# Kernel optimization log

Measured on AMD Instinct MI355X. Metric: run time of the kernel, lower is better.

The kernel has to match this reference:

```python
import jax, jax.numpy as jnp
import numpy as np

# --- static config matching init_kwargs ---
L = 6            # discretization level -> 2^L Euler substeps per unit time
T = 10           # number of time units
N = 1000         # number of particles
DX = 16          # state dim (== obs dim)
INIT_VAL = 0.0
SUB = 2 ** L
HL = 2.0 ** (-L)
S = SUB * T + 1  # total path length


def setup_inputs() -> dict:
    key = jax.random.key(0)
    k1, k2, k3, k4 = jax.random.split(key, 4)
    input_path = jax.random.normal(k1, (S, DX), dtype=jnp.float32) * 0.1
    observe_path = jax.random.normal(k2, (T + 1, DX), dtype=jnp.float32) * 0.5
    # stable linear drift mu(x) = x @ A.T, constant diffusion matrix Sig
    A = (-0.5 * jnp.eye(DX) + 0.05 * jax.random.normal(k3, (DX, DX))).astype(jnp.float32)
    Sig = (0.3 * jnp.eye(DX) + 0.02 * jax.random.normal(k4, (DX, DX))).astype(jnp.float32)
    return {"input_path": input_path, "observe_path": observe_path, "A": A, "Sig": Sig}


def _mu(x, A):
    return x @ A.T


def _llg(x, y):
    # Gaussian observation log-likelihood per particle: x (N,DX), y (DX,)
    return -0.5 * jnp.sum((y - x) ** 2, axis=-1)


def _euler_segment(x0, A, Sig, key):
    # unit_path_update: 2^L Euler-Maruyama steps; returns (SUB, N, DX)
    dw = jax.random.normal(key, (SUB, x0.shape[0], DX)) * np.sqrt(HL).astype(np.float32)
    def step(x, d):
        xn = x + _mu(x, A) * HL + d @ Sig.T
        return xn, xn
    _, seg = jax.lax.scan(step, x0, dw)
    return seg


def _multinomial_idx(wn, dice):
    bins = jnp.cumsum(wn)
    bins = bins.at[-1].set(jnp.maximum(1.0, bins[-1]))  # bins[-1] = max(1, bins[-1])
    return jnp.clip(jnp.searchsorted(bins, dice, side="right"), 0, N - 1)


def _forward(input_path, observe_path, A, Sig):
    key = jax.random.key(42)
    un = jnp.full((S, N, DX), INIT_VAL, dtype=input_path.dtype)
    un_hat = jnp.full((S, N, DX), INIT_VAL, dtype=input_path.dtype)
    gn = jnp.zeros((N,), dtype=input_path.dtype)
    wn = jnp.full((N,), 1.0 / N, dtype=input_path.dtype)
    for t in range(T):  # static unroll over time units (indices are static)
        start, upd = SUB * t, SUB * (t + 1)
        kdw = jax.random.fold_in(key, 2 * t)
        kres = jax.random.fold_in(key, 2 * t + 1)
        un = un.at[: start + 1].set(un_hat[: start + 1])
        seg = _euler_segment(un[start], A, Sig, kdw)
        un = un.at[start + 1 : upd + 1].set(seg)
        un = un.at[:, -1, :].set(input_path)  # pin conditioned path as last particle
        gn = _llg(un[upd], observe_path[t + 1]) + gn
        wn = jax.nn.softmax(gn)  # exp(gn - max)/sum, numerically stable
        ess = 1.0 / jnp.sum(wn ** 2)
        do_rs = ess <= N / 2
        idx = _multinomial_idx(wn, jax.random.uniform(kres, (N,)))
        prefix = un[: upd + 1]
        gathered = prefix[:, idx, :]
        new_prefix = jnp.where(do_rs, gathered, prefix)
        gn = jnp.where(do_rs, jnp.zeros_like(gn), gn)
        un_hat = un_hat.at[: upd + 1].set(new_prefix)
        un_hat = un_hat.at[:, -1, :].set(input_path)
    # sample_output: draw one particle index from final weights
    kfin = jax.random.fold_in(key, 2 * T)
    i0 = _multinomial_idx(wn, jax.random.uniform(kfin, (1,)))[0]
    return un[:, i0, :]  # (S, DX)


def reference(input_path, observe_path, A, Sig):
    return _forward(input_path, observe_path, A, Sig)
```

## Files before the change

### kernel.cpp

```cpp
#include <hip/hip_runtime.h>
#include <cstdint>
#include <cstddef>

#pragma clang fp contract(off)


typedef unsigned int u32;

#define NP   1000
#define DXC  16
#define SUBC 64
#define TC   10
#define SC   641

#define WS_XS   0
#define WS_ANC  160000
#define WS_LIN  170000
#define WS_XF0  170032
#define WS_XF1  186032
#define WS_GN0  202032
#define WS_GN1  203032
#define WS_DSG  204032

__device__ __forceinline__ u32 rotl32(u32 v, u32 d) { return (v << d) | (v >> (32u - d)); }

__device__ __forceinline__ void tf2x32(u32 k0, u32 k1, u32 c0, u32 c1, u32& o0, u32& o1) {
  u32 ks0 = k0, ks1 = k1, ks2 = k0 ^ k1 ^ 0x1BD11BDAu;
  u32 x0 = c0 + ks0, x1 = c1 + ks1;
  x0 += x1; x1 = rotl32(x1,13); x1 ^= x0;
  x0 += x1; x1 = rotl32(x1,15); x1 ^= x0;
  x0 += x1; x1 = rotl32(x1,26); x1 ^= x0;
  x0 += x1; x1 = rotl32(x1, 6); x1 ^= x0;
  x0 += ks1; x1 += ks2 + 1u;
  x0 += x1; x1 = rotl32(x1,17); x1 ^= x0;
  x0 += x1; x1 = rotl32(x1,29); x1 ^= x0;
  x0 += x1; x1 = rotl32(x1,16); x1 ^= x0;
  x0 += x1; x1 = rotl32(x1,24); x1 ^= x0;
  x0 += ks2; x1 += ks0 + 2u;
  x0 += x1; x1 = rotl32(x1,13); x1 ^= x0;
  x0 += x1; x1 = rotl32(x1,15); x1 ^= x0;
  x0 += x1; x1 = rotl32(x1,26); x1 ^= x0;
  x0 += x1; x1 = rotl32(x1, 6); x1 ^= x0;
  x0 += ks0; x1 += ks1 + 3u;
  x0 += x1; x1 = rotl32(x1,17); x1 ^= x0;
  x0 += x1; x1 = rotl32(x1,29); x1 ^= x0;
  x0 += x1; x1 = rotl32(x1,16); x1 ^= x0;
  x0 += x1; x1 = rotl32(x1,24); x1 ^= x0;
  x0 += ks1; x1 += ks2 + 4u;
  x0 += x1; x1 = rotl32(x1,13); x1 ^= x0;
  x0 += x1; x1 = rotl32(x1,15); x1 ^= x0;
  x0 += x1; x1 = rotl32(x1,26); x1 ^= x0;
  x0 += x1; x1 = rotl32(x1, 6); x1 ^= x0;
  x0 += ks2; x1 += ks0 + 5u;
  o0 = x0; o1 = x1;
}

__device__ __forceinline__ u32 bits32p(u32 k0, u32 k1, u32 i) {
  u32 o0, o1; tf2x32(k0, k1, 0u, i, o0, o1); return o0 ^ o1;
}

__device__ __forceinline__ float u01(u32 b) {
  return __uint_as_float((b >> 9) | 0x3f800000u) - 1.0f;
}

__device__ __forceinline__ float xla_exp(float input) {
#pragma clang fp contract(off)
  float x = fminf(input, 88.3762626647950f);
  x = fmaxf(x, -88.3762626647949f);
  float fx = floorf(__builtin_fmaf(x, 1.44269504088896341f, 0.5f));
  float tmp = 0.693359375f * fx;
  float z0  = -2.12194440e-4f * fx;
  float xr = x - tmp;
  xr = xr - z0;
  float z = xr * xr;
  float y = __builtin_fmaf(xr, 1.9875691500e-4f, 1.3981999507e-3f);
  y = __builtin_fmaf(y, xr, 8.3334519073e-3f);
  y = __builtin_fmaf(y, xr, 4.1665795894e-2f);
  y = __builtin_fmaf(y, xr, 1.6666665459e-1f);
  y = __builtin_fmaf(y, xr, 5.0000001201e-1f);
  y = __builtin_fmaf(y, z, xr);
  y = 1.0f + y;
  int n = (int)fx;
  float p2n = __uint_as_float((u32)(n + 127) << 23);
  float res = y * p2n;
  return fmaxf(res, input);
}

__device__ __forceinline__ float xla_log(float input) {
#pragma clang fp contract(off)
  float t0 = fmaxf(input, __uint_as_float(0x00800000u));
  u32 bi = __float_as_uint(t0);
  float e = (float)(int)((bi >> 23) - 126u);
  float x = __uint_as_float((bi & 0x807fffffu) | 0x3f000000u);
  float mo, mx;
  if (x < 0.707106781186547524f) { mx = x; mo = 1.0f; } else { mx = 0.0f; mo = 0.0f; }
  x = x - 1.0f;
  e = e - mo;
  x = x + mx;
  float z = x * x;
  float y = __builtin_fmaf(x, 7.0376836292e-2f, -1.1514610310e-1f);
  y = __builtin_fmaf(y, x, 1.1676998740e-1f);
  y = __builtin_fmaf(y, x, -1.2420140846e-1f);
  y = __builtin_fmaf(y, x, 1.4249322787e-1f);
  y = __builtin_fmaf(y, x, -1.6668057665e-1f);
  y = __builtin_fmaf(y, x, 2.0000714765e-1f);
  y = __builtin_fmaf(y, x, -2.4999993993e-1f);
  y = __builtin_fmaf(y, x, 3.3333331174e-1f);
  y = y * x;
  y = y * z;
  y = __builtin_fmaf(e, -2.12194440e-4f, y);
  y = y - 0.5f * z;
  x = x + y;
  x = __builtin_fmaf(e, 0.693359375f, x);
  return x;
}

__device__ __forceinline__ float xla_log1p(float x) {
#pragma clang fp contract(off)
  float ax = fabsf(x);
  if (ax < 1e-4f) {
    float t = (-0.5f * x) + 1.0f;
    return t * x;
  }
  return xla_log(x + 1.0f);
}

__device__ __forceinline__ float xla_erfinv(float u) {
#pragma clang fp contract(off)
  float w = -xla_log1p((-u) * u);
  float p;
  if (w < 5.0f) {
    float ww = w - 2.5f;
    p = 2.81022636e-08f;
    p = 3.43273939e-07f  + p * ww;
    p = -3.5233877e-06f  + p * ww;
    p = -4.39150654e-06f + p * ww;
    p = 0.00021858087f   + p * ww;
    p = -0.00125372503f  + p * ww;
    p = -0.00417768164f  + p * ww;
    p = 0.246640727f     + p * ww;
    p = 1.50140941f      + p * ww;
  } else {
    float ww = (float)__builtin_sqrt((double)w) - 3.0f;
    p = -0.000200214257f;
    p = 0.000100950558f + p * ww;
    p = 0.00134934322f  + p * ww;
    p = -0.00367342844f + p * ww;
    p = 0.00573950773f  + p * ww;
    p = -0.0076224613f  + p * ww;
    p = 0.00943887047f  + p * ww;
    p = 1.00167406f     + p * ww;
    p = 2.83297682f     + p * ww;
  }
  return p * u;
}

#define U_LO __uint_as_float(0xBF7FFFFFu)

__device__ __forceinline__ float nrm(u32 bits) {
#pragma clang fp contract(off)
  float f = u01(bits);
  float u = (f * 2.0f) + U_LO;
  u = fmaxf(U_LO, u);
  return __uint_as_float(0x3FB504F3u) * xla_erfinv(u);
}

__global__ __launch_bounds__(512, 1) void k_gen(const float* __restrict__ Sg,
                                                float* __restrict__ wsf) {
#pragma clang fp contract(off)
  __shared__ float Sg_s[256];
  int tid = threadIdx.x;
  if (tid < 256) Sg_s[tid] = Sg[tid];
  __syncthreads();
  int gtid = (int)blockIdx.x * 512 + tid;
  int nl = gtid & 7;
  int s  = (gtid >> 3) & 63;
  int q  = gtid >> 9;
  int t  = q / 125, blk = q - t * 125;
  int n  = blk * 8 + nl;
  u32 k0, k1; tf2x32(0u, 42u, 0u, (u32)(2 * t), k0, k1);
  float dwv[DXC];
#pragma unroll
  for (int k = 0; k < DXC; ++k) {
    u32 b = bits32p(k0, k1, (u32)(s * 16000 + n * 16 + k));
    dwv[k] = nrm(b) * 0.125f;
  }
  float* dst = wsf + WS_DSG + (size_t)gtid * 16;
#pragma unroll
  for (int d = 0; d < DXC; ++d) {
    float dg = 0.0f;
#pragma unroll
    for (int k = 0; k < DXC; ++k) dg = __builtin_fmaf(dwv[k], Sg_s[d * 16 + k], dg);
    dst[d] = dg;
  }
}

__device__ void cumsum_tree_par(const float* x0, float* out0, float* scr, int tid) {
#pragma clang fp contract(off)
  const int nlv[10] = {1000, 500, 250, 125, 62, 31, 15, 7, 3, 1};
  const float* raw[10]; float* scn[10]; float* rawm[10];
  raw[0] = x0; scn[0] = out0;
  int off = 0;
  for (int k = 1; k < 10; ++k) {
    rawm[k] = scr + off; raw[k] = rawm[k]; off += nlv[k];
    scn[k] = scr + off; off += nlv[k];
  }
  for (int k = 0; k < 9; ++k) {
    int nr = nlv[k + 1];
    for (int i = tid; i < nr; i += 512) rawm[k + 1][i] = raw[k][2 * i] + raw[k][2 * i + 1];
    __syncthreads();
  }
  if (tid == 0) scn[9][0] = raw[9][0];
  __syncthreads();
  for (int k = 8; k >= 0; --k) {
    int nk = nlv[k], nr = nlv[k + 1];
    if (tid == 0) scn[k][0] = raw[k][0];
    for (int i = tid; i < nr; i += 512) scn[k][2 * i + 1] = scn[k + 1][i];
    if ((nk & 1) == 0) {
      for (int i = 1 + tid; i < nr; i += 512) scn[k][2 * i] = scn[k + 1][i - 1] + raw[k][2 * i];
    } else {
      for (int i = 1 + tid; i <= nr; i += 512) scn[k][2 * i] = scn[k + 1][i - 1] + raw[k][2 * i];
    }
    __syncthreads();
  }
}

__device__ void filter_step(int s, const float* __restrict__ inp,
                            const float* __restrict__ obs,
                            float* __restrict__ wsf, int tid, int wr,
                            float* gn_s, float* e_s, float* wn_s, float* bins_s,
                            float* scr_s, float* red_s, int* src_s, float* sh) {
#pragma clang fp contract(off)
  const float* XFp = wsf + ((s & 1) ? WS_XF1 : WS_XF0);
  const float* GNp = wsf + (((s & 1) ^ 1) ? WS_GN1 : WS_GN0);
  float* GNw = wsf + ((s & 1) ? WS_GN1 : WS_GN0);
  int* ANC = (int*)(wsf + WS_ANC);
  int upd = SUBC * (s + 1);

  for (int n = tid; n < NP; n += 512) {
    float sacc = 0.0f;
    for (int d = 0; d < DXC; ++d) {
      float fv = (n == NP - 1) ? inp[upd * 16 + d] : XFp[n * 16 + d];
      float dd = obs[(s + 1) * 16 + d] - fv;
      float sq = dd * dd;
      sacc = sacc + sq;
    }
    float gp = (s == 0) ? 0.0f : GNp[n];
    gn_s[n] = (-0.5f * sacc) + gp;
  }
  __syncthreads();
  {
    float mv = -__builtin_inff();
    for (int n = tid; n < NP; n += 512) mv = fmaxf(mv, gn_s[n]);
#pragma unroll
    for (int off = 32; off >= 1; off >>= 1) mv = fmaxf(mv, __shfl_xor(mv, off));
    if ((tid & 63) == 0) red_s[tid >> 6] = mv;
    __syncthreads();
    if (tid == 0) {
      float a = fmaxf(fmaxf(red_s[0], red_s[1]), fmaxf(red_s[2], red_s[3]));
      float b = fmaxf(fmaxf(red_s[4], red_s[5]), fmaxf(red_s[6], red_s[7]));
      sh[0] = fmaxf(a, b);
    }
    __syncthreads();
  }
  float m = sh[0];
  for (int n = tid; n < NP; n += 512) e_s[n] = xla_exp(gn_s[n] - m);
  __syncthreads();
  if (tid < 8) {
    float a = 0.0f;
    for (int i = 0; i < 125; ++i) a = a + e_s[i * 8 + tid];
    red_s[tid] = a;
  }
  __syncthreads();
  if (tid == 0) {
    float b0 = red_s[0] + red_s[4], b1 = red_s[1] + red_s[5],
          b2 = red_s[2] + red_s[6], b3 = red_s[3] + red_s[7];
    float c0 = b0 + b2, c1 = b1 + b3;
    sh[1] = c0 + c1;
  }
  __syncthreads();
  float ssum = sh[1];
  for (int n = tid; n < NP; n += 512) wn_s[n] = e_s[n] / ssum;
  __syncthreads();
  if (tid < 8) {
    float a = 0.0f;
    for (int i = 0; i < 125; ++i) { float v = wn_s[i * 8 + tid]; float q = v * v; a = a + q; }
    red_s[tid] = a;
  }
  __syncthreads();
  if (tid == 0) {
    float b0 = red_s[0] + red_s[4], b1 = red_s[1] + red_s[5],
          b2 = red_s[2] + red_s[6], b3 = red_s[3] + red_s[7];
    float c0 = b0 + b2, c1 = b1 + b3;
    float ss = c0 + c1;
    float ess = 1.0f / ss;
    sh[2] = (ess <= 500.0f) ? 1.0f : 0.0f;
  }
  __syncthreads();
  cumsum_tree_par(wn_s, bins_s, scr_s, tid);
  if (tid == 0) bins_s[NP - 1] = fmaxf(1.0f, bins_s[NP - 1]);
  __syncthreads();
  int rs = (sh[2] != 0.0f);
  u32 kr0, kr1; tf2x32(0u, 42u, 0u, (u32)(2 * s + 1), kr0, kr1);
  for (int n = tid; n < NP; n += 512) {
    u32 b = bits32p(kr0, kr1, (u32)n);
    float dice = fmaxf(0.0f, u01(b));
    int lo = 0, hi = NP;
    while (lo < hi) { int mid = (lo + hi) >> 1; if (bins_s[mid] <= dice) lo = mid + 1; else hi = mid; }
    int idx = lo > NP - 1 ? NP - 1 : lo;
    int a = rs ? idx : n;
    src_s[n] = (n == NP - 1) ? (NP - 1) : a;
    if (wr) {
      ANC[s * NP + n] = a;
      GNw[n] = rs ? 0.0f : gn_s[n];
    }
  }
  __syncthreads();
}

__global__ __launch_bounds__(512, 1) void k_step(const float* __restrict__ inp,
                                                 const float* __restrict__ obs,
                                                 const float* __restrict__ A,
                                                 float* __restrict__ wsf, int t) {
#pragma clang fp contract(off)
  __shared__ float dsg_s[8192];
  __shared__ float gn_s[NP], e_s[NP], wn_s[NP], bins_s[NP], scr_s[2048];
  __shared__ float red_s[8], sh[4];
  __shared__ int src_s[NP];
  int tid = threadIdx.x;
  int base = (int)blockIdx.x * 8;
  const float* DSG = wsf + WS_DSG + (size_t)t * 1024000 + (size_t)blockIdx.x * 8192;
#pragma unroll
  for (int j = 0; j < 16; ++j) dsg_s[j * 512 + tid] = DSG[j * 512 + tid];
  if (t > 0) {
    filter_step(t - 1, inp, obs, wsf, tid, blockIdx.x == 0,
                gn_s, e_s, wn_s, bins_s, scr_s, red_s, src_s, sh);
  } else {
    __syncthreads();
  }
  if (tid < 128) {
    int p = tid >> 4, d = tid & 15;
    int n = base + p;
    float Ar[DXC];
#pragma unroll
    for (int k = 0; k < DXC; ++k) Ar[k] = A[d * 16 + k];
    float x = 0.0f;
    if (t > 0) {
      const float* XFp = wsf + (((t - 1) & 1) ? WS_XF1 : WS_XF0);
      int s0 = src_s[n];
      x = (s0 == NP - 1) ? inp[(SUBC * t) * 16 + d] : XFp[s0 * 16 + d];
    }
    wsf[WS_XS + t * 16000 + n * 16 + d] = x;
    for (int sl = 0; sl < SUBC; ++sl) {
      float mu = 0.0f;
#pragma unroll
      for (int k = 0; k < DXC; ++k) {
        float xk = __shfl(x, k, 16);
        mu = __builtin_fmaf(xk, Ar[k], mu);
      }
      float t2 = x + mu * 0.015625f;
      x = t2 + dsg_s[sl * 128 + p * 16 + d];
    }
    float* XFc = wsf + ((t & 1) ? WS_XF1 : WS_XF0);
    XFc[n * 16 + d] = x;
  }
}

__global__ __launch_bounds__(512, 1) void k_fin(const float* __restrict__ inp,
                                                const float* __restrict__ obs,
                                                float* __restrict__ wsf) {
#pragma clang fp contract(off)
  __shared__ float gn_s[NP], e_s[NP], wn_s[NP], bins_s[NP], scr_s[2048];
  __shared__ float red_s[8], sh[4];
  __shared__ int src_s[NP];
  int tid = threadIdx.x;
  filter_step(TC - 1, inp, obs, wsf, tid, 0,
              gn_s, e_s, wn_s, bins_s, scr_s, red_s, src_s, sh);
  if (tid == 0) {
    const int* ANC = (const int*)(wsf + WS_ANC);
    int* LIN = (int*)(wsf + WS_LIN);
    u32 kf0, kf1; tf2x32(0u, 42u, 0u, (u32)(2 * TC), kf0, kf1);
    u32 b = bits32p(kf0, kf1, 0u);
    float dice = fmaxf(0.0f, u01(b));
    int lo = 0, hi = NP;
    while (lo < hi) { int mid = (lo + hi) >> 1; if (bins_s[mid] <= dice) lo = mid + 1; else hi = mid; }
    int i0 = lo > NP - 1 ? NP - 1 : lo;
    LIN[0] = i0;
    LIN[1 + 9] = i0;
    int hit = (i0 == NP - 1) ? 1 : 0;
    LIN[11 + 9] = hit;
    int j = i0;
    for (int u = 8; u >= 0; --u) {
      j = ANC[u * NP + j];
      if (j == NP - 1) hit = 1;
      LIN[1 + u] = j;
      LIN[11 + u] = hit;
    }
  }
}

__global__ __launch_bounds__(256, 1) void k_out(const float* __restrict__ inp,
                                                const float* __restrict__ A,
                                                const float* __restrict__ wsf,
                                                float* __restrict__ out) {
#pragma clang fp contract(off)
  __shared__ float dsg_t[1024];
  __shared__ int lin_s[24];
  const int* LIN = (const int*)(wsf + WS_LIN);
  int tid = threadIdx.x;
  int bid = (int)blockIdx.x;
  if (tid < 24) lin_s[tid] = LIN[tid];
  __syncthreads();
  int i0 = lin_s[0];
  int i = bid * 256 + tid;
  if (i < SC * DXC) {
    int srow = i >> 4;
    if (i0 == NP - 1) out[i] = inp[i];
    else if (srow == 0) out[i] = lin_s[11 + 0] ? inp[i] : 0.0f;
    else { int u = (srow - 1) >> 6; if (lin_s[11 + u]) out[i] = inp[i]; }
  }
  if (bid >= TC) return;
  if (i0 == NP - 1) return;
  int u = bid;
  if (lin_s[11 + u]) return;
  int p = lin_s[1 + u];
  const float* DSG = wsf + WS_DSG + (size_t)u * 1024000 + (size_t)(p >> 3) * 8192
                     + (size_t)(p & 7) * 16;
#pragma unroll
  for (int j = 0; j < 4; ++j) {
    int idx = j * 256 + tid;
    int sl = idx >> 4, d = idx & 15;
    dsg_t[idx] = DSG[sl * 128 + d];
  }
  __syncthreads();
  if (tid < 16) {
    int d = tid;
    float Ar[DXC];
#pragma unroll
    for (int k = 0; k < DXC; ++k) Ar[k] = A[d * 16 + k];
    float x = wsf[WS_XS + u * 16000 + p * 16 + d];
    for (int sl = 0; sl < SUBC; ++sl) {
      float mu = 0.0f;
#pragma unroll
      for (int k = 0; k < DXC; ++k) {
        float xk = __shfl(x, k, 16);
        mu = __builtin_fmaf(xk, Ar[k], mu);
      }
      float t2 = x + mu * 0.015625f;
      x = t2 + dsg_t[sl * 16 + d];
      out[(u * SUBC + sl + 1) * DXC + d] = x;
    }
  }
}

extern "C" void kernel_launch(void* const* d_in, const int* in_sizes, int n_in,
                              void* d_out, int out_size, void* d_ws, size_t ws_size,
                              hipStream_t stream) {
  (void)in_sizes; (void)n_in; (void)out_size; (void)ws_size;
  const float* inp = (const float*)d_in[0];
  const float* obs = (const float*)d_in[1];
  const float* A   = (const float*)d_in[2];
  const float* Sg  = (const float*)d_in[3];
  float* wsf = (float*)d_ws;
  float* out = (float*)d_out;

  k_gen<<<dim3(1250), dim3(512), 0, stream>>>(Sg, wsf);
  for (int t = 0; t < TC; ++t) {
    k_step<<<dim3(125), dim3(512), 0, stream>>>(inp, obs, A, wsf, t);
  }
  k_fin<<<dim3(1), dim3(512), 0, stream>>>(inp, obs, wsf);
  k_out<<<dim3(41), dim3(256), 0, stream>>>(inp, A, wsf, out);
}
```

Before: 344.5 us.

## Overlap noise generation with step kernels and merge final filter into output kernel

The upfront noise-generation kernel for all time units is split up. Only unit 0 is generated first, and each step kernel launches 125 extra blocks that generate the noise for the next time unit while the 125 filter blocks run. The single-block final filter kernel is merged into the output kernel, with every block redundantly recomputing the final resampling and lineage into shared memory. This removes one launch and the lineage round-trip through global memory. In exchange, k_out blocks repeat the filter_step work, and step kernels use more blocks.

Measured after the change: 311.3 us. 1.11x faster.

```diff
diff --git a/kernel.cpp b/kernel.cpp
--- a/kernel.cpp
+++ b/kernel.cpp
@@ -15,7 +15,6 @@
 
 #define WS_XS   0
 #define WS_ANC  160000
-#define WS_LIN  170000
 #define WS_XF0  170032
 #define WS_XF1  186032
 #define WS_GN0  202032
@@ -165,19 +164,14 @@
   return __uint_as_float(0x3FB504F3u) * xla_erfinv(u);
 }
 
-__global__ __launch_bounds__(512, 1) void k_gen(const float* __restrict__ Sg,
-                                                float* __restrict__ wsf) {
-#pragma clang fp contract(off)
-  __shared__ float Sg_s[256];
-  int tid = threadIdx.x;
-  if (tid < 256) Sg_s[tid] = Sg[tid];
-  __syncthreads();
-  int gtid = (int)blockIdx.x * 512 + tid;
-  int nl = gtid & 7;
-  int s  = (gtid >> 3) & 63;
-  int q  = gtid >> 9;
-  int t  = q / 125, blk = q - t * 125;
+__device__ __forceinline__ void gen_unit(int t, int blk, int tid,
+                                         const float* __restrict__ Sg_s,
+                                         float* __restrict__ wsf) {
+#pragma clang fp contract(off)
+  int nl = tid & 7;
+  int s  = tid >> 3;
   int n  = blk * 8 + nl;
+  int gtid = (t * 125 + blk) * 512 + tid;
   u32 k0, k1; tf2x32(0u, 42u, 0u, (u32)(2 * t), k0, k1);
   float dwv[DXC];
 #pragma unroll
@@ -318,9 +312,19 @@
   __syncthreads();
 }
 
+__global__ __launch_bounds__(512, 1) void k_gen0(const float* __restrict__ Sg,
+                                                 float* __restrict__ wsf) {
+  __shared__ float Sg_s[256];
+  int tid = threadIdx.x;
+  if (tid < 256) Sg_s[tid] = Sg[tid];
+  __syncthreads();
+  gen_unit(0, (int)blockIdx.x, tid, Sg_s, wsf);
+}
+
 __global__ __launch_bounds__(512, 1) void k_step(const float* __restrict__ inp,
                                                  const float* __restrict__ obs,
                                                  const float* __restrict__ A,
+                                                 const float* __restrict__ Sg,
                                                  float* __restrict__ wsf, int t) {
 #pragma clang fp contract(off)
   __shared__ float dsg_s[8192];
@@ -328,12 +332,21 @@
   __shared__ float red_s[8], sh[4];
   __shared__ int src_s[NP];
   int tid = threadIdx.x;
-  int base = (int)blockIdx.x * 8;
-  const float* DSG = wsf + WS_DSG + (size_t)t * 1024000 + (size_t)blockIdx.x * 8192;
+  int bid = (int)blockIdx.x;
+  if (bid >= 125) {
+    if (t >= TC - 1) return;
+    __shared__ float Sg_s[256];
+    if (tid < 256) Sg_s[tid] = Sg[tid];
+    __syncthreads();
+    gen_unit(t + 1, bid - 125, tid, Sg_s, wsf);
+    return;
+  }
+  int base = bid * 8;
+  const float* DSG = wsf + WS_DSG + (size_t)t * 1024000 + (size_t)bid * 8192;
 #pragma unroll
   for (int j = 0; j < 16; ++j) dsg_s[j * 512 + tid] = DSG[j * 512 + tid];
   if (t > 0) {
-    filter_step(t - 1, inp, obs, wsf, tid, blockIdx.x == 0,
+    filter_step(t - 1, inp, obs, wsf, tid, bid == 0,
                 gn_s, e_s, wn_s, bins_s, scr_s, red_s, src_s, sh);
   } else {
     __syncthreads();
@@ -366,53 +379,44 @@
   }
 }
 
-__global__ __launch_bounds__(512, 1) void k_fin(const float* __restrict__ inp,
+__global__ __launch_bounds__(512, 1) void k_out(const float* __restrict__ inp,
                                                 const float* __restrict__ obs,
-                                                float* __restrict__ wsf) {
+                                                const float* __restrict__ A,
+                                                float* __restrict__ wsf,
+                                                float* __restrict__ out) {
 #pragma clang fp contract(off)
   __shared__ float gn_s[NP], e_s[NP], wn_s[NP], bins_s[NP], scr_s[2048];
   __shared__ float red_s[8], sh[4];
   __shared__ int src_s[NP];
+  __shared__ float dsg_t[1024];
+  __shared__ int lin_s[24];
   int tid = threadIdx.x;
+  int bid = (int)blockIdx.x;
   filter_step(TC - 1, inp, obs, wsf, tid, 0,
               gn_s, e_s, wn_s, bins_s, scr_s, red_s, src_s, sh);
   if (tid == 0) {
     const int* ANC = (const int*)(wsf + WS_ANC);
-    int* LIN = (int*)(wsf + WS_LIN);
     u32 kf0, kf1; tf2x32(0u, 42u, 0u, (u32)(2 * TC), kf0, kf1);
     u32 b = bits32p(kf0, kf1, 0u);
     float dice = fmaxf(0.0f, u01(b));
     int lo = 0, hi = NP;
     while (lo < hi) { int mid = (lo + hi) >> 1; if (bins_s[mid] <= dice) lo = mid + 1; else hi = mid; }
     int i0 = lo > NP - 1 ? NP - 1 : lo;
-    LIN[0] = i0;
-    LIN[1 + 9] = i0;
+    lin_s[0] = i0;
+    lin_s[1 + 9] = i0;
     int hit = (i0 == NP - 1) ? 1 : 0;
-    LIN[11 + 9] = hit;
+    lin_s[11 + 9] = hit;
     int j = i0;
     for (int u = 8; u >= 0; --u) {
       j = ANC[u * NP + j];
       if (j == NP - 1) hit = 1;
-      LIN[1 + u] = j;
-      LIN[11 + u] = hit;
-    }
-  }
-}
-
-__global__ __launch_bounds__(256, 1) void k_out(const float* __restrict__ inp,
-                                                const float* __restrict__ A,
-                                                const float* __restrict__ wsf,
-                                                float* __restrict__ out) {
-#pragma clang fp contract(off)
-  __shared__ float dsg_t[1024];
-  __shared__ int lin_s[24];
-  const int* LIN = (const int*)(wsf + WS_LIN);
-  int tid = threadIdx.x;
-  int bid = (int)blockIdx.x;
-  if (tid < 24) lin_s[tid] = LIN[tid];
+      lin_s[1 + u] = j;
+      lin_s[11 + u] = hit;
+    }
+  }
   __syncthreads();
   int i0 = lin_s[0];
-  int i = bid * 256 + tid;
+  int i = bid * 512 + tid;
   if (i < SC * DXC) {
     int srow = i >> 4;
     if (i0 == NP - 1) out[i] = inp[i];
@@ -426,10 +430,12 @@
   int p = lin_s[1 + u];
   const float* DSG = wsf + WS_DSG + (size_t)u * 1024000 + (size_t)(p >> 3) * 8192
                      + (size_t)(p & 7) * 16;
-#pragma unroll
-  for (int j = 0; j < 4; ++j) {
-    int idx = j * 256 + tid;
+  {
+    int idx = tid;
     int sl = idx >> 4, d = idx & 15;
+    dsg_t[idx] = DSG[sl * 128 + d];
+    idx = 512 + tid;
+    sl = idx >> 4; d = idx & 15;
     dsg_t[idx] = DSG[sl * 128 + d];
   }
   __syncthreads();
@@ -464,10 +470,9 @@
   float* wsf = (float*)d_ws;
   float* out = (float*)d_out;
 
-  k_gen<<<dim3(1250), dim3(512), 0, stream>>>(Sg, wsf);
+  k_gen0<<<dim3(125), dim3(512), 0, stream>>>(Sg, wsf);
   for (int t = 0; t < TC; ++t) {
-    k_step<<<dim3(125), dim3(512), 0, stream>>>(inp, obs, A, wsf, t);
-  }
-  k_fin<<<dim3(1), dim3(512), 0, stream>>>(inp, obs, wsf);
-  k_out<<<dim3(41), dim3(256), 0, stream>>>(inp, A, wsf, out);
-}
+    k_step<<<dim3(250), dim3(512), 0, stream>>>(inp, obs, A, Sg, wsf, t);
+  }
+  k_out<<<dim3(21), dim3(512), 0, stream>>>(inp, obs, A, wsf, out);
+}
```
